# Optimization experiments

Hardware: AMD Instinct MI355X
Metric: run time of the kernel (lower is better)

## Reference

```python
import jax, jax.numpy as jnp
import numpy as np

EMBED_DIM = 1024
NUM_HEADS = 16
HEAD_DIM = EMBED_DIM // NUM_HEADS


def setup_inputs() -> dict:
    key = jax.random.key(0)
    k1, k2, k3, k4, k5 = jax.random.split(key, 5)
    B, N, D = 2, 2048, EMBED_DIM
    s = 1.0 / np.sqrt(D)
    x = jax.random.normal(k1, (B, N, D), dtype=jnp.float32)
    qkv_w = jax.random.uniform(k2, (3 * D, D), minval=-s, maxval=s, dtype=jnp.float32)
    qkv_b = jax.random.uniform(k3, (3 * D,), minval=-s, maxval=s, dtype=jnp.float32)
    proj_w = jax.random.uniform(k4, (D, D), minval=-s, maxval=s, dtype=jnp.float32)
    proj_b = jax.random.uniform(k5, (D,), minval=-s, maxval=s, dtype=jnp.float32)
    return {"x": x, "qkv_w": qkv_w, "qkv_b": qkv_b, "proj_w": proj_w, "proj_b": proj_b}


def reference(x, qkv_w, qkv_b, proj_w, proj_b):
    B, N, D = x.shape
    H, Hd = NUM_HEADS, HEAD_DIM
    scale = Hd ** (-0.5)
    # QKV projection (torch Linear: x @ W.T + b)
    qkv = x @ qkv_w.T + qkv_b                      # [B, N, 3D]
    q, k, v = jnp.split(qkv, 3, axis=-1)
    def split_heads(t):
        return t.reshape(B, N, H, Hd).transpose(0, 2, 1, 3)  # [B, H, N, Hd]
    q, k, v = map(split_heads, (q, k, v))
    attn = jnp.einsum("bhqd,bhkd->bhqk", q, k) * scale       # [B, H, N, N]
    attn = jax.nn.softmax(attn, axis=-1)
    out = jnp.einsum("bhqk,bhkd->bhqd", attn, v)             # [B, H, N, Hd]
    out = out.transpose(0, 2, 1, 3).reshape(B, N, D)
    return out @ proj_w.T + proj_b
```

## Files before the change

### kernel.cpp

```cpp
#include <hip/hip_runtime.h>
#include <hip/hip_bf16.h>


#define DEV __device__ __forceinline__

typedef __attribute__((ext_vector_type(8))) __bf16 bf16x8;
typedef __attribute__((ext_vector_type(4))) float f32x4;

static DEV unsigned short f2bf(float f) {
  unsigned u = __builtin_bit_cast(unsigned, f);
  u += 0x7FFFu + ((u >> 16) & 1u);
  return (unsigned short)(u >> 16);
}

static DEV unsigned pkhalfup(float lo, float hi) {
  unsigned a = __builtin_bit_cast(unsigned, lo) + 0x8000u;
  unsigned b = __builtin_bit_cast(unsigned, hi) + 0x8000u;
  return (a >> 16) | (b & 0xFFFF0000u);
}

static DEV float fexp2(float x) {
#if __has_builtin(__builtin_amdgcn_exp2f)
  return __builtin_amdgcn_exp2f(x);
#else
  return __expf(x * 0.69314718055994531f);
#endif
}

static DEV float max3(float a, float b, float c) {
  return fmaxf(fmaxf(a, b), c);
}

static DEV void gld16(const void* g, void* l) {
  __builtin_amdgcn_global_load_lds(
      (const __attribute__((address_space(1))) unsigned int*)g,
      (__attribute__((address_space(3))) unsigned int*)l, 16, 0, 0);
}

static DEV f32x4 mfma16(bf16x8 a, bf16x8 b, f32x4 c) {
  return __builtin_amdgcn_mfma_f32_16x16x32_bf16(a, b, c, 0, 0, 0);
}

__global__ void k_conv(const float* __restrict__ x, const float* __restrict__ qw,
                       const float* __restrict__ pw, unsigned short* __restrict__ xb,
                       unsigned short* __restrict__ wqb, unsigned short* __restrict__ pwb) {
  int b = blockIdx.x;
  const float* s;
  unsigned short* d;
  int base;
  if (b < 4096)      { s = x;  d = xb;  base = b; }
  else if (b < 7168) { s = qw; d = wqb; base = b - 4096; }
  else               { s = pw; d = pwb; base = b - 7168; }
  int i = (base * 256 + threadIdx.x) * 4;
  float4 v = *reinterpret_cast<const float4*>(s + i);
  union { unsigned short h[4]; uint2 u; } cv;
  cv.h[0] = f2bf(v.x); cv.h[1] = f2bf(v.y); cv.h[2] = f2bf(v.z); cv.h[3] = f2bf(v.w);
  *reinterpret_cast<uint2*>(d + i) = cv.u;
}

static DEV void gemm_tile(const unsigned short* __restrict__ Asb,
                          const unsigned short* __restrict__ Bsb,
                          int wm, int wn, int fr, int fg, f32x4 (&acc)[4][4]) {
  bf16x8 af[4], bw[4];
#pragma unroll
  for (int m = 0; m < 4; ++m)
    af[m] = *reinterpret_cast<const bf16x8*>(Asb + (wm * 64 + m * 16 + fr) * 32 + fg * 8);
#pragma unroll
  for (int n = 0; n < 4; ++n)
    bw[n] = *reinterpret_cast<const bf16x8*>(Bsb + (wn * 64 + n * 16 + fr) * 32 + fg * 8);
#pragma unroll
  for (int m = 0; m < 4; ++m)
#pragma unroll
    for (int n = 0; n < 4; ++n)
      acc[m][n] = mfma16(af[m], bw[n], acc[m][n]);
}

#define QSTAGE(k0)                                                            \
  {                                                                           \
    _Pragma("unroll")                                                         \
    for (int c = 0; c < 2; ++c) {                                             \
      int bi = c * 4096 + wid * 1024 + lane * 16;                             \
      int row = bi >> 6, ce = (bi & 63) >> 1;                                 \
      gld16(gA + (size_t)row * K + (k0) + ce, As + c * 2048 + wid * 512);     \
      gld16(gW + (size_t)row * K + (k0) + ce, Bs + c * 2048 + wid * 512);     \
    }                                                                         \
  }

__global__ __launch_bounds__(256) void k_qkv(
    const unsigned short* __restrict__ A, const unsigned short* __restrict__ W,
    const float* __restrict__ bias, unsigned short* __restrict__ Qb,
    unsigned short* __restrict__ Kb, unsigned short* __restrict__ Vt) {
  const int K = 1024;
  __shared__ __align__(16) unsigned short As[128 * 32], Bs[128 * 32];
  const int tid = threadIdx.x, lane = tid & 63, wid = tid >> 6;
  const int wm = wid >> 1, wn = wid & 1, fr = lane & 15, fg = lane >> 4;
  const size_t bm = blockIdx.x, bn = blockIdx.y;
  const unsigned short* gA = A + bm * 128 * K;
  const unsigned short* gW = W + bn * 128 * K;
  f32x4 acc[4][4] = {};
  for (int k0 = 0; k0 < K; k0 += 32) {
    QSTAGE(k0);
    __syncthreads();
    gemm_tile(As, Bs, wm, wn, fr, fg, acc);
    __syncthreads();
  }
  const float QSCALE = 0.18033688011112043f;
  float bv[4];
#pragma unroll
  for (int n = 0; n < 4; ++n) bv[n] = bias[bn * 128 + wn * 64 + n * 16 + fr];
#pragma unroll
  for (int m = 0; m < 4; ++m)
#pragma unroll
    for (int n = 0; n < 4; ++n) {
      int f = (int)bn * 128 + wn * 64 + n * 16 + fr;
      int t = f >> 10, d = f & 1023, h = d >> 6, hd = d & 63;
      int token0 = (int)bm * 128 + wm * 64 + m * 16 + fg * 4;
      int b_ = token0 >> 11, nn0 = token0 & 2047;
      size_t bh = (size_t)(b_ * 16 + h);
      float v0 = acc[m][n][0] + bv[n], v1 = acc[m][n][1] + bv[n];
      float v2 = acc[m][n][2] + bv[n], v3 = acc[m][n][3] + bv[n];
      if (t == 0) {
        unsigned short* q = Qb + (bh * 2048 + nn0) * 64 + hd;
        q[0] = f2bf(v0 * QSCALE); q[64] = f2bf(v1 * QSCALE);
        q[128] = f2bf(v2 * QSCALE); q[192] = f2bf(v3 * QSCALE);
      } else if (t == 1) {
        unsigned short* k = Kb + (bh * 2048 + nn0) * 64 + hd;
        k[0] = f2bf(v0); k[64] = f2bf(v1); k[128] = f2bf(v2); k[192] = f2bf(v3);
      } else {
        union { unsigned short h[4]; uint2 u; } pk;
        pk.h[0] = f2bf(v0); pk.h[1] = f2bf(v1);
        pk.h[2] = f2bf(v2); pk.h[3] = f2bf(v3);
        *reinterpret_cast<uint2*>(Vt + (bh * 64 + hd) * 2048 + nn0) = pk.u;
      }
    }
}

static DEV void attn_tile(const unsigned short* __restrict__ Ksb,
                          const unsigned short* __restrict__ Vsb,
                          unsigned short* __restrict__ pw, const bf16x8* qf,
                          int fr, int fg, const int* kcol, const int* pcol,
                          f32x4* accO, float& mrow, float& lpart) {
  const int prow = fr * 64;
  f32x4 s[4] = {};
  __builtin_amdgcn_s_setprio(1);
#pragma unroll
  for (int nf = 0; nf < 4; ++nf)
#pragma unroll
    for (int ks = 0; ks < 2; ++ks) {
      bf16x8 kf = *reinterpret_cast<const bf16x8*>(&Ksb[(nf * 16 + fr) * 64 + kcol[ks]]);
      s[nf] = mfma16(kf, qf[ks], s[nf]);
    }
  __builtin_amdgcn_s_setprio(0);
  bf16x8 vf[2][4];
#pragma unroll
  for (int ks = 0; ks < 2; ++ks)
#pragma unroll
    for (int df = 0; df < 4; ++df)
      vf[ks][df] = *reinterpret_cast<const bf16x8*>(&Vsb[(df * 16 + fr) * 64 + kcol[ks]]);
  float m0 = max3(s[0][0], s[0][1], s[0][2]);
  float m1 = max3(s[0][3], s[1][0], s[1][1]);
  float m2 = max3(s[1][2], s[1][3], s[2][0]);
  float m3 = max3(s[2][1], s[2][2], s[2][3]);
  float m4 = max3(s[3][0], s[3][1], s[3][2]);
  float mymax = fmaxf(max3(m0, m1, m2), max3(m3, m4, s[3][3]));
  if (!__all(mymax <= mrow + 8.0f)) {
    float pmax = fmaxf(mymax, __shfl_xor(mymax, 16));
    pmax = fmaxf(pmax, __shfl_xor(pmax, 32));
    float mnew = fmaxf(mrow, pmax);
    float sc = fexp2(mrow - mnew);
    mrow = mnew;
    lpart *= sc;
    float scq[4];
#pragma unroll
    for (int r = 0; r < 4; ++r) scq[r] = __shfl(sc, fg * 4 + r);
#pragma unroll
    for (int df = 0; df < 4; ++df)
#pragma unroll
      for (int r = 0; r < 4; ++r) accO[df][r] *= scq[r];
  }
  float rsn[4];
#pragma unroll
  for (int nf = 0; nf < 4; ++nf) {
    float p0 = fexp2(s[nf][0] - mrow), p1 = fexp2(s[nf][1] - mrow);
    float p2 = fexp2(s[nf][2] - mrow), p3 = fexp2(s[nf][3] - mrow);
    uint2 pk;
    pk.x = pkhalfup(p0, p1);
    pk.y = pkhalfup(p2, p3);
    rsn[nf] = (p0 + p1) + (p2 + p3);
    *reinterpret_cast<uint2*>(&pw[prow + pcol[nf]]) = pk;
  }
  lpart += (rsn[0] + rsn[1]) + (rsn[2] + rsn[3]);
  bf16x8 pf[2];
#pragma unroll
  for (int ks = 0; ks < 2; ++ks)
    pf[ks] = *reinterpret_cast<const bf16x8*>(&pw[prow + kcol[ks]]);
  __builtin_amdgcn_s_setprio(1);
#pragma unroll
  for (int df = 0; df < 4; ++df)
#pragma unroll
    for (int ks = 0; ks < 2; ++ks)
      accO[df] = mfma16(pf[ks], vf[ks][df], accO[df]);
  __builtin_amdgcn_s_setprio(0);
}

__global__ __launch_bounds__(256) void k_attn(
    const unsigned short* __restrict__ Qb, const unsigned short* __restrict__ Kb,
    const unsigned short* __restrict__ Vt, unsigned short* __restrict__ Ob) {
  __shared__ __align__(16) unsigned short Ks0[64 * 64], Ks1[64 * 64];
  __shared__ __align__(16) unsigned short Vs0[64 * 64], Vs1[64 * 64];
  __shared__ __align__(16) unsigned short p_lds[4][16 * 64];
  const int tid = threadIdx.x, lane = tid & 63, w = tid >> 6;
  const int fr = lane & 15, fg = lane >> 4;
  const int bid = (int)(blockIdx.x & 7) * 128 + (int)(blockIdx.x >> 3);
  const int qt = bid & 31, bh = bid >> 5;
  const unsigned short* Qp = Qb + ((size_t)bh * 2048 + qt * 64 + w * 16) * 64;
  const unsigned short* Kp = Kb + (size_t)bh * 2048 * 64;
  const unsigned short* Vp = Vt + (size_t)bh * 64 * 2048;
  unsigned short* pw = &p_lds[w][0];

  int kcol[2], pcol[4];
#pragma unroll
  for (int ks = 0; ks < 2; ++ks) kcol[ks] = ((ks * 4 + fg) ^ (fr & 7)) * 8;
#pragma unroll
  for (int nf = 0; nf < 4; ++nf)
    pcol[nf] = (((2 * nf + (fg >> 1)) ^ (fr & 7)) * 8) + (fg & 1) * 4;

  const int crow0 = w * 16 + (lane >> 3);
  bf16x8 qf[2];
#pragma unroll
  for (int ks = 0; ks < 2; ++ks)
    qf[ks] = *reinterpret_cast<const bf16x8*>(Qp + fr * 64 + ks * 32 + fg * 8);

  f32x4 accO[4] = {};
  float mrow = -1e30f, lpart = 0.f;

#define STAGE(KDST, VDST, kti)                                                \
  {                                                                           \
    const unsigned short* Kt_ = Kp + (kti) * 64 * 64;                         \
    _Pragma("unroll")                                                         \
    for (int j = 0; j < 2; ++j) {                                             \
      int cr = crow0 + j * 8;                                                 \
      int cs = (lane & 7) ^ (cr & 7);                                         \
      gld16(Kt_ + cr * 64 + cs * 8, (KDST) + (w * 2 + j) * 512);              \
      gld16(Vp + (size_t)cr * 2048 + (kti) * 64 + cs * 8,                     \
            (VDST) + (w * 2 + j) * 512);                                      \
    }                                                                         \
  }

  STAGE(Ks0, Vs0, 0);
  STAGE(Ks1, Vs1, 1);
  __syncthreads();
  for (int i = 0; i < 16; ++i) {
    attn_tile(Ks0, Vs0, pw, qf, fr, fg, kcol, pcol, accO, mrow, lpart);
    __syncthreads();
    if (i < 15) STAGE(Ks0, Vs0, 2 * i + 2);
    attn_tile(Ks1, Vs1, pw, qf, fr, fg, kcol, pcol, accO, mrow, lpart);
    __syncthreads();
    if (i < 15) STAGE(Ks1, Vs1, 2 * i + 3);
  }
#undef STAGE
  float lrow = lpart;
  lrow += __shfl_xor(lrow, 16);
  lrow += __shfl_xor(lrow, 32);
  float linv = 1.f / lrow;
  float lq[4];
#pragma unroll
  for (int r = 0; r < 4; ++r) lq[r] = __shfl(linv, fg * 4 + r);
  const int b_ = bh >> 4, h = bh & 15;
#pragma unroll
  for (int df = 0; df < 4; ++df)
#pragma unroll
    for (int r = 0; r < 4; ++r) {
      int nn = qt * 64 + w * 16 + fg * 4 + r;
      int d = df * 16 + fr;
      Ob[(size_t)(b_ * 2048 + nn) * 1024 + h * 64 + d] = f2bf(accO[df][r] * lq[r]);
    }
}

__global__ __launch_bounds__(256) void k_proj(
    const unsigned short* __restrict__ A, const unsigned short* __restrict__ W,
    const float* __restrict__ bias, float* __restrict__ out) {
  const int K = 1024;
  __shared__ __align__(16) unsigned short As[128 * 32], Bs[128 * 32];
  const int tid = threadIdx.x, lane = tid & 63, wid = tid >> 6;
  const int wm = wid >> 1, wn = wid & 1, fr = lane & 15, fg = lane >> 4;
  const size_t bm = blockIdx.x, bn = blockIdx.y;
  const unsigned short* gA = A + bm * 128 * K;
  const unsigned short* gW = W + bn * 128 * K;
  f32x4 acc[4][4] = {};
  for (int k0 = 0; k0 < K; k0 += 32) {
    QSTAGE(k0);
    __syncthreads();
    gemm_tile(As, Bs, wm, wn, fr, fg, acc);
    __syncthreads();
  }
  float bv[4];
#pragma unroll
  for (int n = 0; n < 4; ++n) bv[n] = bias[bn * 128 + wn * 64 + n * 16 + fr];
#pragma unroll
  for (int m = 0; m < 4; ++m)
#pragma unroll
    for (int n = 0; n < 4; ++n)
#pragma unroll
      for (int r = 0; r < 4; ++r) {
        size_t token = bm * 128 + wm * 64 + m * 16 + fg * 4 + r;
        int f = (int)bn * 128 + wn * 64 + n * 16 + fr;
        out[token * 1024 + f] = acc[m][n][r] + bv[n];
      }
}

extern "C" void kernel_launch(void* const* d_in, const int* in_sizes, int n_in,
                              void* d_out, int out_size, void* d_ws, size_t ws_size,
                              hipStream_t stream) {
  const float* x      = (const float*)d_in[0];
  const float* qkv_w  = (const float*)d_in[1];
  const float* qkv_b  = (const float*)d_in[2];
  const float* proj_w = (const float*)d_in[3];
  const float* proj_b = (const float*)d_in[4];
  float* out = (float*)d_out;
  char* ws = (char*)d_ws;
  unsigned short* xb  = (unsigned short*)(ws);
  unsigned short* wqb = (unsigned short*)(ws + (size_t)(8u << 20));
  unsigned short* pwb = (unsigned short*)(ws + (size_t)(14u << 20));
  unsigned short* Qb  = (unsigned short*)(ws + (size_t)(16u << 20));
  unsigned short* Kb  = (unsigned short*)(ws + (size_t)(24u << 20));
  unsigned short* Vt  = (unsigned short*)(ws + (size_t)(32u << 20));
  unsigned short* Ob  = (unsigned short*)(ws + (size_t)(40u << 20));

  k_conv<<<8192, 256, 0, stream>>>(x, qkv_w, proj_w, xb, wqb, pwb);
  k_qkv<<<dim3(32, 24), 256, 0, stream>>>(xb, wqb, qkv_b, Qb, Kb, Vt);
  k_attn<<<1024, 256, 0, stream>>>(Qb, Kb, Vt, Ob);
  k_proj<<<dim3(32, 8), 256, 0, stream>>>(Ob, pwb, proj_b, out);
}
```

Baseline: 202.3 us.

## Process two 16-row query fragments per wave in attention kernel

Each wave now handles 32 query rows (two 16-row fragments) instead of 16, so a block covers 128 queries and the grid halves to 512 blocks. Each K fragment loaded from LDS feeds two MFMAs, and each staged K/V tile is reused by twice as many queries, which cuts LDS reads and global K/V traffic per query. The cost is more registers for the doubled accumulators and scores, and fewer blocks (512 on 256 CUs), which may lower occupancy and latency hiding.

```diff
diff --git a/kernel.cpp b/kernel.cpp
--- a/kernel.cpp
+++ b/kernel.cpp
@@ -137,18 +137,21 @@
 
 static DEV void attn_tile(const unsigned short* __restrict__ Ksb,
                           const unsigned short* __restrict__ Vsb,
-                          unsigned short* __restrict__ pw, const bf16x8* qf,
-                          int fr, int fg, const int* kcol, const int* pcol,
-                          f32x4* accO, float& mrow, float& lpart) {
+                          unsigned short* __restrict__ pw,
+                          const bf16x8 (&qf)[2][2], int fr, int fg,
+                          const int* kcol, const int* pcol,
+                          f32x4 (&accO)[2][4], float (&mrow)[2],
+                          float (&lpart)[2]) {
   const int prow = fr * 64;
-  f32x4 s[4] = {};
+  f32x4 s[2][4] = {};
   __builtin_amdgcn_s_setprio(1);
 #pragma unroll
   for (int nf = 0; nf < 4; ++nf)
 #pragma unroll
     for (int ks = 0; ks < 2; ++ks) {
       bf16x8 kf = *reinterpret_cast<const bf16x8*>(&Ksb[(nf * 16 + fr) * 64 + kcol[ks]]);
-      s[nf] = mfma16(kf, qf[ks], s[nf]);
+      s[0][nf] = mfma16(kf, qf[0][ks], s[0][nf]);
+      s[1][nf] = mfma16(kf, qf[1][ks], s[1][nf]);
     }
   __builtin_amdgcn_s_setprio(0);
   bf16x8 vf[2][4];
@@ -157,50 +160,53 @@
 #pragma unroll
     for (int df = 0; df < 4; ++df)
       vf[ks][df] = *reinterpret_cast<const bf16x8*>(&Vsb[(df * 16 + fr) * 64 + kcol[ks]]);
-  float m0 = max3(s[0][0], s[0][1], s[0][2]);
-  float m1 = max3(s[0][3], s[1][0], s[1][1]);
-  float m2 = max3(s[1][2], s[1][3], s[2][0]);
-  float m3 = max3(s[2][1], s[2][2], s[2][3]);
-  float m4 = max3(s[3][0], s[3][1], s[3][2]);
-  float mymax = fmaxf(max3(m0, m1, m2), max3(m3, m4, s[3][3]));
-  if (!__all(mymax <= mrow + 8.0f)) {
-    float pmax = fmaxf(mymax, __shfl_xor(mymax, 16));
-    pmax = fmaxf(pmax, __shfl_xor(pmax, 32));
-    float mnew = fmaxf(mrow, pmax);
-    float sc = fexp2(mrow - mnew);
-    mrow = mnew;
-    lpart *= sc;
-    float scq[4];
-#pragma unroll
-    for (int r = 0; r < 4; ++r) scq[r] = __shfl(sc, fg * 4 + r);
+#pragma unroll
+  for (int m = 0; m < 2; ++m) {
+    float m0 = max3(s[m][0][0], s[m][0][1], s[m][0][2]);
+    float m1 = max3(s[m][0][3], s[m][1][0], s[m][1][1]);
+    float m2 = max3(s[m][1][2], s[m][1][3], s[m][2][0]);
+    float m3 = max3(s[m][2][1], s[m][2][2], s[m][2][3]);
+    float m4 = max3(s[m][3][0], s[m][3][1], s[m][3][2]);
+    float mymax = fmaxf(max3(m0, m1, m2), max3(m3, m4, s[m][3][3]));
+    if (!__all(mymax <= mrow[m] + 8.0f)) {
+      float pmax = fmaxf(mymax, __shfl_xor(mymax, 16));
+      pmax = fmaxf(pmax, __shfl_xor(pmax, 32));
+      float mnew = fmaxf(mrow[m], pmax);
+      float sc = fexp2(mrow[m] - mnew);
+      mrow[m] = mnew;
+      lpart[m] *= sc;
+      float scq[4];
+#pragma unroll
+      for (int r = 0; r < 4; ++r) scq[r] = __shfl(sc, fg * 4 + r);
+#pragma unroll
+      for (int df = 0; df < 4; ++df)
+#pragma unroll
+        for (int r = 0; r < 4; ++r) accO[m][df][r] *= scq[r];
+    }
+    float rsn[4];
+#pragma unroll
+    for (int nf = 0; nf < 4; ++nf) {
+      float p0 = fexp2(s[m][nf][0] - mrow[m]), p1 = fexp2(s[m][nf][1] - mrow[m]);
+      float p2 = fexp2(s[m][nf][2] - mrow[m]), p3 = fexp2(s[m][nf][3] - mrow[m]);
+      uint2 pk;
+      pk.x = pkhalfup(p0, p1);
+      pk.y = pkhalfup(p2, p3);
+      rsn[nf] = (p0 + p1) + (p2 + p3);
+      *reinterpret_cast<uint2*>(&pw[prow + pcol[nf]]) = pk;
+    }
+    lpart[m] += (rsn[0] + rsn[1]) + (rsn[2] + rsn[3]);
+    bf16x8 pf[2];
+#pragma unroll
+    for (int ks = 0; ks < 2; ++ks)
+      pf[ks] = *reinterpret_cast<const bf16x8*>(&pw[prow + kcol[ks]]);
+    __builtin_amdgcn_s_setprio(1);
 #pragma unroll
     for (int df = 0; df < 4; ++df)
 #pragma unroll
-      for (int r = 0; r < 4; ++r) accO[df][r] *= scq[r];
-  }
-  float rsn[4];
-#pragma unroll
-  for (int nf = 0; nf < 4; ++nf) {
-    float p0 = fexp2(s[nf][0] - mrow), p1 = fexp2(s[nf][1] - mrow);
-    float p2 = fexp2(s[nf][2] - mrow), p3 = fexp2(s[nf][3] - mrow);
-    uint2 pk;
-    pk.x = pkhalfup(p0, p1);
-    pk.y = pkhalfup(p2, p3);
-    rsn[nf] = (p0 + p1) + (p2 + p3);
-    *reinterpret_cast<uint2*>(&pw[prow + pcol[nf]]) = pk;
-  }
-  lpart += (rsn[0] + rsn[1]) + (rsn[2] + rsn[3]);
-  bf16x8 pf[2];
-#pragma unroll
-  for (int ks = 0; ks < 2; ++ks)
-    pf[ks] = *reinterpret_cast<const bf16x8*>(&pw[prow + kcol[ks]]);
-  __builtin_amdgcn_s_setprio(1);
-#pragma unroll
-  for (int df = 0; df < 4; ++df)
-#pragma unroll
-    for (int ks = 0; ks < 2; ++ks)
-      accO[df] = mfma16(pf[ks], vf[ks][df], accO[df]);
-  __builtin_amdgcn_s_setprio(0);
+      for (int ks = 0; ks < 2; ++ks)
+        accO[m][df] = mfma16(pf[ks], vf[ks][df], accO[m][df]);
+    __builtin_amdgcn_s_setprio(0);
+  }
 }
 
 __global__ __launch_bounds__(256) void k_attn(
@@ -211,9 +217,9 @@
   __shared__ __align__(16) unsigned short p_lds[4][16 * 64];
   const int tid = threadIdx.x, lane = tid & 63, w = tid >> 6;
   const int fr = lane & 15, fg = lane >> 4;
-  const int bid = (int)(blockIdx.x & 7) * 128 + (int)(blockIdx.x >> 3);
-  const int qt = bid & 31, bh = bid >> 5;
-  const unsigned short* Qp = Qb + ((size_t)bh * 2048 + qt * 64 + w * 16) * 64;
+  const int bid = (int)(blockIdx.x & 7) * 64 + (int)(blockIdx.x >> 3);
+  const int qt = bid & 15, bh = bid >> 4;
+  const unsigned short* Qp = Qb + ((size_t)bh * 2048 + qt * 128 + w * 32) * 64;
   const unsigned short* Kp = Kb + (size_t)bh * 2048 * 64;
   const unsigned short* Vp = Vt + (size_t)bh * 64 * 2048;
   unsigned short* pw = &p_lds[w][0];
@@ -226,13 +232,16 @@
     pcol[nf] = (((2 * nf + (fg >> 1)) ^ (fr & 7)) * 8) + (fg & 1) * 4;
 
   const int crow0 = w * 16 + (lane >> 3);
-  bf16x8 qf[2];
-#pragma unroll
-  for (int ks = 0; ks < 2; ++ks)
-    qf[ks] = *reinterpret_cast<const bf16x8*>(Qp + fr * 64 + ks * 32 + fg * 8);
-
-  f32x4 accO[4] = {};
-  float mrow = -1e30f, lpart = 0.f;
+  bf16x8 qf[2][2];
+#pragma unroll
+  for (int m = 0; m < 2; ++m)
+#pragma unroll
+    for (int ks = 0; ks < 2; ++ks)
+      qf[m][ks] = *reinterpret_cast<const bf16x8*>(
+          Qp + (m * 16 + fr) * 64 + ks * 32 + fg * 8);
+
+  f32x4 accO[2][4] = {};
+  float mrow[2] = {-1e30f, -1e30f}, lpart[2] = {0.f, 0.f};
 
 #define STAGE(KDST, VDST, kti)                                                \
   {                                                                           \
@@ -259,22 +268,26 @@
     if (i < 15) STAGE(Ks1, Vs1, 2 * i + 3);
   }
 #undef STAGE
-  float lrow = lpart;
-  lrow += __shfl_xor(lrow, 16);
-  lrow += __shfl_xor(lrow, 32);
-  float linv = 1.f / lrow;
-  float lq[4];
-#pragma unroll
-  for (int r = 0; r < 4; ++r) lq[r] = __shfl(linv, fg * 4 + r);
   const int b_ = bh >> 4, h = bh & 15;
 #pragma unroll
-  for (int df = 0; df < 4; ++df)
-#pragma unroll
-    for (int r = 0; r < 4; ++r) {
-      int nn = qt * 64 + w * 16 + fg * 4 + r;
-      int d = df * 16 + fr;
-      Ob[(size_t)(b_ * 2048 + nn) * 1024 + h * 64 + d] = f2bf(accO[df][r] * lq[r]);
-    }
+  for (int m = 0; m < 2; ++m) {
+    float lrow = lpart[m];
+    lrow += __shfl_xor(lrow, 16);
+    lrow += __shfl_xor(lrow, 32);
+    float linv = 1.f / lrow;
+    float lq[4];
+#pragma unroll
+    for (int r = 0; r < 4; ++r) lq[r] = __shfl(linv, fg * 4 + r);
+#pragma unroll
+    for (int df = 0; df < 4; ++df)
+#pragma unroll
+      for (int r = 0; r < 4; ++r) {
+        int nn = qt * 128 + w * 32 + m * 16 + fg * 4 + r;
+        int d = df * 16 + fr;
+        Ob[(size_t)(b_ * 2048 + nn) * 1024 + h * 64 + d] =
+            f2bf(accO[m][df][r] * lq[r]);
+      }
+  }
 }
 
 __global__ __launch_bounds__(256) void k_proj(
@@ -329,6 +342,6 @@
 
   k_conv<<<8192, 256, 0, stream>>>(x, qkv_w, proj_w, xb, wqb, pwb);
   k_qkv<<<dim3(32, 24), 256, 0, stream>>>(xb, wqb, qkv_b, Qb, Kb, Vt);
-  k_attn<<<1024, 256, 0, stream>>>(Qb, Kb, Vt, Ob);
+  k_attn<<<512, 256, 0, stream>>>(Qb, Kb, Vt, Ob);
   k_proj<<<dim3(32, 8), 256, 0, stream>>>(Ob, pwb, proj_b, out);
 }
```

Result: faster. 194.4 us (-3.9%).
